# Performance work log

Hardware: AMD Instinct MI355X
Metric: run time of the kernel (lower is better)

Reference implementation:

```python
import jax, jax.numpy as jnp
import numpy as np

N_NODES = 20000
N_EDGES = 320000
IN_DIM = 128
HID = 64
LATENT = 32
NUM_GRAPHS = 64
NEG_SLOPE = 0.2
BN_EPS = 1e-5


def setup_inputs() -> dict:
    key = jax.random.key(0)
    ks = jax.random.split(key, 24)
    def glorot(k, shape):
        fan_in, fan_out = shape[0], shape[-1]
        lim = (6.0 / (fan_in + fan_out)) ** 0.5
        return jax.random.uniform(k, shape, jnp.float32, -lim, lim)
    inp = {
        "x": jax.random.normal(ks[0], (N_NODES, IN_DIM), jnp.float32),
        "edge_index": jax.random.randint(ks[1], (2, N_EDGES), 0, N_NODES, jnp.int64),
        "batch": jnp.sort(jax.random.randint(ks[2], (N_NODES,), 0, NUM_GRAPHS, jnp.int64)),
        # layer 0: in=128 -> out=64, heads=4
        "Wl0": glorot(ks[3], (IN_DIM, 4 * HID)),
        "Wr0": glorot(ks[4], (IN_DIM, 4 * HID)),
        "att0": glorot(ks[5], (4, HID)),
        "b0": jnp.zeros((4 * HID,), jnp.float32),
        # layer 1: in=256 -> out=64, heads=4
        "Wl1": glorot(ks[6], (4 * HID, 4 * HID)),
        "Wr1": glorot(ks[7], (4 * HID, 4 * HID)),
        "att1": glorot(ks[8], (4, HID)),
        "b1": jnp.zeros((4 * HID,), jnp.float32),
        # layer 2: in=256 -> out=64, heads=1
        "Wl2": glorot(ks[9], (4 * HID, HID)),
        "Wr2": glorot(ks[10], (4 * HID, HID)),
        "att2": glorot(ks[11], (1, HID)),
        "b2": jnp.zeros((HID,), jnp.float32),
        # BatchNorm1d(hidden_dim) in eval mode (running stats)
        "bn_gamma": jax.random.uniform(ks[12], (HID,), jnp.float32, 0.5, 1.5),
        "bn_beta": jax.random.normal(ks[13], (HID,), jnp.float32) * 0.1,
        "bn_mean": jax.random.normal(ks[14], (HID,), jnp.float32) * 0.1,
        "bn_var": jax.random.uniform(ks[15], (HID,), jnp.float32, 0.5, 1.5),
        # fc: hidden -> latent
        "fc_w": glorot(ks[16], (HID, LATENT)),
        "fc_b": jnp.zeros((LATENT,), jnp.float32),
    }
    return inp


def gatv2_layer(h, src, dst, Wl, Wr, att, bias):
    # PyG GATv2Conv (concat=True, negative_slope=0.2, self loops already in src/dst)
    N = h.shape[0]
    H, C = att.shape
    xl = (h @ Wl).reshape(N, H, C)  # source transform
    xr = (h @ Wr).reshape(N, H, C)  # target transform
    e = jax.nn.leaky_relu(xl[src] + xr[dst], NEG_SLOPE)   # [E,H,C]
    logits = jnp.einsum("ehc,hc->eh", e, att)             # [E,H]
    # softmax over incoming edges per destination node
    m = jax.ops.segment_max(logits, dst, num_segments=N)  # [N,H]
    ex = jnp.exp(logits - m[dst])
    denom = jax.ops.segment_sum(ex, dst, num_segments=N)
    alpha = ex / denom[dst]                               # [E,H]
    out = jax.ops.segment_sum(alpha[:, :, None] * xl[src], dst, num_segments=N)
    return out.reshape(N, H * C) + bias


def reference(x, edge_index, batch, Wl0, Wr0, att0, b0, Wl1, Wr1, att1, b1,
              Wl2, Wr2, att2, b2, bn_gamma, bn_beta, bn_mean, bn_var, fc_w, fc_b):
    N = x.shape[0]
    loop = jnp.arange(N, dtype=edge_index.dtype)
    src = jnp.concatenate([edge_index[0], loop])  # add self loops (PyG default)
    dst = jnp.concatenate([edge_index[1], loop])
    h = gatv2_layer(x, src, dst, Wl0, Wr0, att0, b0)   # dropout: eval mode -> identity
    h = gatv2_layer(h, src, dst, Wl1, Wr1, att1, b1)
    h = gatv2_layer(h, src, dst, Wl2, Wr2, att2, b2)   # [N, HID]
    pooled = jax.ops.segment_sum(h, batch, num_segments=NUM_GRAPHS)  # global_add_pool
    bn = (pooled - bn_mean) * jax.lax.rsqrt(bn_var + BN_EPS) * bn_gamma + bn_beta
    return bn @ fc_w + fc_b  # [NUM_GRAPHS, LATENT]
```

## Files before the change

kernel.cpp:

```cpp
#include <hip/hip_runtime.h>
#include <math.h>

#define N_NODES 20000
#define E_ORIG  320000
#define E_TOT   340000
#define NUM_GRAPHS 64
#define NCHUNK 10
#define NBINS (N_NODES * NCHUNK)
#define SCAN_BLOCKS 196

typedef __attribute__((ext_vector_type(8))) short bf16x8;
typedef __attribute__((ext_vector_type(4))) float f32x4;

__device__ __forceinline__ ushort f2bf(float x) {
  unsigned u = __float_as_uint(x);
  return (ushort)((u + 0x7fffu + ((u >> 16) & 1u)) >> 16);
}
__device__ __forceinline__ float4 ld_bf16x4(const ushort* p) {
  ushort4 u = *(const ushort4*)p;
  float4 f;
  f.x = __uint_as_float((unsigned)u.x << 16);
  f.y = __uint_as_float((unsigned)u.y << 16);
  f.z = __uint_as_float((unsigned)u.z << 16);
  f.w = __uint_as_float((unsigned)u.w << 16);
  return f;
}
__device__ __forceinline__ void gl_lds16(const void* g, void* l) {
  __builtin_amdgcn_global_load_lds(
      (const __attribute__((address_space(1))) unsigned*)(uintptr_t)g,
      (__attribute__((address_space(3))) unsigned*)(uintptr_t)l, 16, 0, 0);
}

__global__ __launch_bounds__(256) void prep(
    const float* __restrict__ x,
    const float* __restrict__ Wl0, const float* __restrict__ Wr0,
    const float* __restrict__ Wl1, const float* __restrict__ Wr1,
    const float* __restrict__ Wl2, const float* __restrict__ Wr2,
    ushort* __restrict__ x16, ushort* __restrict__ Bt0,
    ushort* __restrict__ Bt1, ushort* __restrict__ Bt2, int* __restrict__ deg)
{
  const int Z0 = 640000;
  const int Z1 = Z0 + 65536;
  const int Z2 = Z1 + 131072;
  const int Z3 = Z2 + 32768;
  const int Z4 = Z3 + NBINS / 4;
  int t = blockIdx.x * 256 + threadIdx.x;
  if (t < Z0) {
    int i = t << 2;
    float4 v = *(const float4*)&x[i];
    ushort4 o; o.x = f2bf(v.x); o.y = f2bf(v.y); o.z = f2bf(v.z); o.w = f2bf(v.w);
    *(ushort4*)&x16[i] = o;
  } else if (t < Z1) {
    int idx = t - Z0; int n = idx >> 7, k = idx & 127;
    float v = (n < 256) ? Wl0[k * 256 + n] : Wr0[k * 256 + (n - 256)];
    Bt0[idx] = f2bf(v);
  } else if (t < Z2) {
    int idx = t - Z1; int n = idx >> 8, k = idx & 255;
    float v = (n < 256) ? Wl1[k * 256 + n] : Wr1[k * 256 + (n - 256)];
    Bt1[idx] = f2bf(v);
  } else if (t < Z3) {
    int idx = t - Z2; int n = idx >> 8, k = idx & 255;
    float v = (n < 64) ? Wl2[k * 64 + n] : Wr2[k * 64 + (n - 64)];
    Bt2[idx] = f2bf(v);
  } else if (t < Z4) {
    int4 z = {0, 0, 0, 0};
    *(int4*)&deg[(t - Z3) << 2] = z;
  }
}


__global__ __launch_bounds__(256) void deg_count(
    const int* __restrict__ esrc, const int* __restrict__ edst,
    int* __restrict__ deg)
{
  int e = blockIdx.x * 256 + threadIdx.x;
  if (e >= E_TOT) return;
  int src, dst;
  if (e < E_ORIG) { src = esrc[e]; dst = edst[e]; }
  else            { src = dst = e - E_ORIG; }
  atomicAdd(&deg[dst * NCHUNK + (src >> 11)], 1);
}

__global__ __launch_bounds__(256) void scan1(
    const int* __restrict__ deg, int* __restrict__ bsum)
{
  __shared__ int red[256];
  const int t = threadIdx.x;
  int base = (blockIdx.x << 10) + (t << 2);
  int s = 0;
  if (base + 4 <= NBINS) {
    int4 v = *(const int4*)&deg[base];
    s = v.x + v.y + v.z + v.w;
  }
  red[t] = s;
  __syncthreads();
  #pragma unroll
  for (int off = 128; off > 0; off >>= 1) {
    if (t < off) red[t] += red[t + off];
    __syncthreads();
  }
  if (t == 0) bsum[blockIdx.x] = red[0];
}

__global__ __launch_bounds__(256) void scan3(
    const int* __restrict__ deg, const int* __restrict__ bsum,
    int* __restrict__ rowptr, int* __restrict__ cursor)
{
  __shared__ int sc[256];
  __shared__ int bs[256];
  const int t = threadIdx.x;
  bs[t] = (t < SCAN_BLOCKS) ? bsum[t] : 0;
  __syncthreads();
  #pragma unroll
  for (int off = 1; off < 256; off <<= 1) {
    int v = (t >= off) ? bs[t - off] : 0;
    __syncthreads();
    bs[t] += v;
    __syncthreads();
  }
  const int myoff = (blockIdx.x == 0) ? 0 : bs[blockIdx.x - 1];

  int base = (blockIdx.x << 10) + (t << 2);
  int4 v = {0, 0, 0, 0};
  if (base + 4 <= NBINS) v = *(const int4*)&deg[base];
  int s = v.x + v.y + v.z + v.w;
  sc[t] = s;
  __syncthreads();
  #pragma unroll
  for (int off = 1; off < 256; off <<= 1) {
    int u = (t >= off) ? sc[t - off] : 0;
    __syncthreads();
    sc[t] += u;
    __syncthreads();
  }
  if (base + 4 <= NBINS) {
    int p = myoff + ((t == 0) ? 0 : sc[t - 1]);
    int4 r;
    r.x = p; r.y = p + v.x; r.z = r.y + v.y; r.w = r.z + v.z;
    *(int4*)&rowptr[base] = r;
    *(int4*)&cursor[base] = r;
  }
  if (blockIdx.x == SCAN_BLOCKS - 1 && t == 255) rowptr[NBINS] = bs[255];
}

__global__ __launch_bounds__(256) void csr_fill(
    const int* __restrict__ esrc, const int* __restrict__ edst,
    int* __restrict__ cursor, int* __restrict__ csr_src)
{
  int e = blockIdx.x * 256 + threadIdx.x;
  if (e >= E_TOT) return;
  int src, dst;
  if (e < E_ORIG) { src = esrc[e]; dst = edst[e]; }
  else            { src = dst = e - E_ORIG; }
  int pos = atomicAdd(&cursor[dst * NCHUNK + (src >> 11)], 1);
  csr_src[pos] = src;
}

__global__ __launch_bounds__(256) void mfma_gemm_bf16(
    const ushort* __restrict__ A, const ushort* __restrict__ Bt,
    ushort* __restrict__ Cl, ushort* __restrict__ Cr, int M, int K, int N)
{
  __shared__ char smem[36864];
  ushort* As = (ushort*)smem;
  ushort* Bs = As + 8192;

  const int mtiles = (M + 127) >> 7;
  const int bid = blockIdx.x;
  const int xcd = bid & 7;
  const int i = bid >> 3;
  const int n0 = (i / 20) << 7;
  const int m = xcd + ((i % 20) << 3);
  if (m >= mtiles) return;
  const int m0 = m << 7;

  const int tid = threadIdx.x;
  const int lane = tid & 63;
  const int w = tid >> 6;
  const int wm = (w >> 1) << 6;
  const int wn = (w & 1) << 6;
  const int quad = lane >> 4;
  const int l15 = lane & 15;

  f32x4 acc[4][4] = {};

  for (int k0 = 0; k0 < K; k0 += 64) {
    #pragma unroll
    for (int r = 0; r < 4; r++) {
      int c = (r << 8) + tid;
      int row = c >> 3;
      int col = (c & 7) << 3;
      int ga = m0 + row; if (ga >= M) ga = M - 1;
      gl_lds16(A  + (size_t)ga * K + k0 + col, (char*)As + c * 16);
      gl_lds16(Bt + (size_t)(n0 + row) * K + k0 + col, (char*)Bs + c * 16);
    }
    __syncthreads();
    #pragma unroll
    for (int ks = 0; ks < 2; ks++) {
      bf16x8 af[4], bfr[4];
      #pragma unroll
      for (int ii = 0; ii < 4; ii++)
        af[ii]  = *(const bf16x8*)&As[(wm + (ii << 4) + l15) * 64 + (ks << 5) + (quad << 3)];
      #pragma unroll
      for (int j = 0; j < 4; j++)
        bfr[j] = *(const bf16x8*)&Bs[(wn + (j << 4) + l15) * 64 + (ks << 5) + (quad << 3)];
      #pragma unroll
      for (int ii = 0; ii < 4; ii++)
        #pragma unroll
        for (int j = 0; j < 4; j++)
          acc[ii][j] = __builtin_amdgcn_mfma_f32_16x16x32_bf16(
              af[ii], bfr[j], acc[ii][j], 0, 0, 0);
    }
    __syncthreads();
  }

  const int halfN = N >> 1;
  const int gc0 = n0 + wn;
  ushort* Cd = (gc0 < halfN) ? Cl : Cr;
  const int cb = (gc0 < halfN) ? gc0 : gc0 - halfN;

  ushort* Cs = (ushort*)smem + w * 4608;
  #pragma unroll
  for (int ii = 0; ii < 4; ii++)
    #pragma unroll
    for (int j = 0; j < 4; j++)
      #pragma unroll
      for (int r = 0; r < 4; r++)
        Cs[((ii << 4) + (quad << 2) + r) * 72 + (j << 4) + l15] = f2bf(acc[ii][j][r]);
  #pragma unroll
  for (int it = 0; it < 8; it++) {
    int row = (it << 3) + (lane >> 3);
    int cc = lane & 7;
    bf16x8 v = *(const bf16x8*)&Cs[row * 72 + (cc << 3)];
    int grow = m0 + wm + row;
    if (grow < M)
      *(bf16x8*)&Cd[(size_t)grow * halfN + cb + (cc << 3)] = v;
  }
}

__device__ __forceinline__ void h4_term(
    float4 xlv, const float4& xrv, const float4& attv, float& v)
{
  float4 a;
  a.x = xlv.x + xrv.x; a.y = xlv.y + xrv.y;
  a.z = xlv.z + xrv.z; a.w = xlv.w + xrv.w;
  a.x = fmaxf(a.x, 0.2f * a.x); a.y = fmaxf(a.y, 0.2f * a.y);
  a.z = fmaxf(a.z, 0.2f * a.z); a.w = fmaxf(a.w, 0.2f * a.w);
  v = a.x * attv.x + a.y * attv.y + a.z * attv.z + a.w * attv.w;
}

__device__ __forceinline__ void h4_edge(
    const float4& xv, const float4& xrv, const float4& attv,
    float4& acc, float& lsum)
{
  float v;
  h4_term(xv, xrv, attv, v);
  v += __shfl_xor(v, 1);
  v += __shfl_xor(v, 2);
  v += __shfl_xor(v, 4);
  v += __shfl_xor(v, 8);
  float w = __expf(v);
  lsum += w;
  acc.x += w * xv.x; acc.y += w * xv.y;
  acc.z += w * xv.z; acc.w += w * xv.w;
}

__global__ __launch_bounds__(256) void gat_gather_h4(
    const ushort* __restrict__ xl16, const ushort* __restrict__ xr16,
    const float* __restrict__ att, const float* __restrict__ bias,
    const int* __restrict__ rowptr, const int* __restrict__ csr_src,
    ushort* __restrict__ hout)
{
  const int n = blockIdx.x * 4 + (threadIdx.x >> 6);
  const int lane = threadIdx.x & 63;
  const int c4 = lane << 2;
  const float4 xrv  = ld_bf16x4(xr16 + (size_t)n * 256 + c4);
  const float4 attv = *(const float4*)&att[c4];
  const int beg = rowptr[n * NCHUNK], end = rowptr[n * NCHUNK + NCHUNK];
  float4 acc = make_float4(0.f, 0.f, 0.f, 0.f);
  float lsum = 0.f;
  int p = beg;
  for (; p + 7 < end; p += 8) {
    int s0 = csr_src[p],     s1 = csr_src[p + 1];
    int s2 = csr_src[p + 2], s3 = csr_src[p + 3];
    int s4 = csr_src[p + 4], s5 = csr_src[p + 5];
    int s6 = csr_src[p + 6], s7 = csr_src[p + 7];
    float4 x0 = ld_bf16x4(xl16 + (size_t)s0 * 256 + c4);
    float4 x1 = ld_bf16x4(xl16 + (size_t)s1 * 256 + c4);
    float4 x2 = ld_bf16x4(xl16 + (size_t)s2 * 256 + c4);
    float4 x3 = ld_bf16x4(xl16 + (size_t)s3 * 256 + c4);
    float4 x4 = ld_bf16x4(xl16 + (size_t)s4 * 256 + c4);
    float4 x5 = ld_bf16x4(xl16 + (size_t)s5 * 256 + c4);
    float4 x6 = ld_bf16x4(xl16 + (size_t)s6 * 256 + c4);
    float4 x7 = ld_bf16x4(xl16 + (size_t)s7 * 256 + c4);
    h4_edge(x0, xrv, attv, acc, lsum);
    h4_edge(x1, xrv, attv, acc, lsum);
    h4_edge(x2, xrv, attv, acc, lsum);
    h4_edge(x3, xrv, attv, acc, lsum);
    h4_edge(x4, xrv, attv, acc, lsum);
    h4_edge(x5, xrv, attv, acc, lsum);
    h4_edge(x6, xrv, attv, acc, lsum);
    h4_edge(x7, xrv, attv, acc, lsum);
  }
  for (; p + 3 < end; p += 4) {
    int s0 = csr_src[p],     s1 = csr_src[p + 1];
    int s2 = csr_src[p + 2], s3 = csr_src[p + 3];
    float4 x0 = ld_bf16x4(xl16 + (size_t)s0 * 256 + c4);
    float4 x1 = ld_bf16x4(xl16 + (size_t)s1 * 256 + c4);
    float4 x2 = ld_bf16x4(xl16 + (size_t)s2 * 256 + c4);
    float4 x3 = ld_bf16x4(xl16 + (size_t)s3 * 256 + c4);
    h4_edge(x0, xrv, attv, acc, lsum);
    h4_edge(x1, xrv, attv, acc, lsum);
    h4_edge(x2, xrv, attv, acc, lsum);
    h4_edge(x3, xrv, attv, acc, lsum);
  }
  for (; p < end; p++) {
    int s0 = csr_src[p];
    float4 x0 = ld_bf16x4(xl16 + (size_t)s0 * 256 + c4);
    h4_edge(x0, xrv, attv, acc, lsum);
  }
  const float4 bv = *(const float4*)&bias[c4];
  float inv = 1.f / lsum;
  ushort4 o;
  o.x = f2bf(acc.x * inv + bv.x); o.y = f2bf(acc.y * inv + bv.y);
  o.z = f2bf(acc.z * inv + bv.z); o.w = f2bf(acc.w * inv + bv.w);
  *(ushort4*)&hout[(size_t)n * 256 + c4] = o;
}

__global__ __launch_bounds__(256) void gat_gather_h1(
    const ushort* __restrict__ xl2, const ushort* __restrict__ xr2,
    const float* __restrict__ att, const float* __restrict__ bias,
    const int* __restrict__ rowptr, const int* __restrict__ csr_src,
    float* __restrict__ h3)
{
  const int n = blockIdx.x * 4 + (threadIdx.x >> 6);
  const int lane = threadIdx.x & 63;
  const int g = lane >> 4, c4 = (lane & 15) << 2;
  const float4 xrv  = ld_bf16x4(xr2 + (size_t)n * 64 + c4);
  const float4 attv = *(const float4*)&att[c4];
  const int beg = rowptr[n * NCHUNK], end = rowptr[n * NCHUNK + NCHUNK];
  float4 acc = make_float4(0.f, 0.f, 0.f, 0.f);
  float lsum = 0.f;
  int p = beg + g;
  for (; p + 4 < end; p += 8) {
    int s0 = csr_src[p], s1 = csr_src[p + 4];
    float4 x0 = ld_bf16x4(xl2 + (size_t)s0 * 64 + c4);
    float4 x1 = ld_bf16x4(xl2 + (size_t)s1 * 64 + c4);
    h4_edge(x0, xrv, attv, acc, lsum);
    h4_edge(x1, xrv, attv, acc, lsum);
  }
  if (p < end) {
    int s0 = csr_src[p];
    float4 x0 = ld_bf16x4(xl2 + (size_t)s0 * 64 + c4);
    h4_edge(x0, xrv, attv, acc, lsum);
  }
  #pragma unroll
  for (int off = 16; off <= 32; off <<= 1) {
    lsum  += __shfl_xor(lsum, off);
    acc.x += __shfl_xor(acc.x, off); acc.y += __shfl_xor(acc.y, off);
    acc.z += __shfl_xor(acc.z, off); acc.w += __shfl_xor(acc.w, off);
  }
  if (g == 0) {
    const float4 bv = *(const float4*)&bias[c4];
    float inv = 1.f / lsum;
    float4 o;
    o.x = acc.x * inv + bv.x; o.y = acc.y * inv + bv.y;
    o.z = acc.z * inv + bv.z; o.w = acc.w * inv + bv.w;
    *(float4*)&h3[(size_t)n * 64 + c4] = o;
  }
}

__global__ __launch_bounds__(256) void pool_bn_fc(
    const float* __restrict__ h3, const int* __restrict__ batch,
    const float* __restrict__ gamma, const float* __restrict__ beta,
    const float* __restrict__ mean, const float* __restrict__ var,
    const float* __restrict__ fcw, const float* __restrict__ fcb,
    float* __restrict__ out)
{
  __shared__ float red[256];
  __shared__ float s[64];
  const int g = blockIdx.x;
  const int t = threadIdx.x;
  const int c = t & 63, r = t >> 6;
  int lo = 0, hi = N_NODES;
  while (lo < hi) { int mid = (lo + hi) >> 1; if (batch[mid] < g) lo = mid + 1; else hi = mid; }
  int s0 = lo;
  hi = N_NODES;
  while (lo < hi) { int mid = (lo + hi) >> 1; if (batch[mid] < g + 1) lo = mid + 1; else hi = mid; }
  int e0 = lo;
  float a = 0.f;
  for (int n = s0 + r; n < e0; n += 4) a += h3[(size_t)n * 64 + c];
  red[t] = a;
  __syncthreads();
  if (r == 0) {
    float p = red[c] + red[c + 64] + red[c + 128] + red[c + 192];
    s[c] = (p - mean[c]) * rsqrtf(var[c] + 1e-5f) * gamma[c] + beta[c];
  }
  __syncthreads();
  if (t < 32) {
    float acc = fcb[t];
    #pragma unroll
    for (int k = 0; k < 64; k++) acc += s[k] * fcw[k * 32 + t];
    out[g * 32 + t] = acc;
  }
}

extern "C" void kernel_launch(void* const* d_in, const int* in_sizes, int n_in,
                              void* d_out, int out_size, void* d_ws, size_t ws_size,
                              hipStream_t stream) {
  const float* x    = (const float*)d_in[0];
  const int*   ei   = (const int*)d_in[1];
  const int*   batch= (const int*)d_in[2];
  const float* Wl0  = (const float*)d_in[3];
  const float* Wr0  = (const float*)d_in[4];
  const float* att0 = (const float*)d_in[5];
  const float* b0   = (const float*)d_in[6];
  const float* Wl1  = (const float*)d_in[7];
  const float* Wr1  = (const float*)d_in[8];
  const float* att1 = (const float*)d_in[9];
  const float* b1   = (const float*)d_in[10];
  const float* Wl2  = (const float*)d_in[11];
  const float* Wr2  = (const float*)d_in[12];
  const float* att2 = (const float*)d_in[13];
  const float* b2   = (const float*)d_in[14];
  const float* bng  = (const float*)d_in[15];
  const float* bnb  = (const float*)d_in[16];
  const float* bnm  = (const float*)d_in[17];
  const float* bnv  = (const float*)d_in[18];
  const float* fcw  = (const float*)d_in[19];
  const float* fcb  = (const float*)d_in[20];
  float* out = (float*)d_out;

  const int* esrc = ei;
  const int* edst = ei + E_ORIG;

  char* w = (char*)d_ws;
  ushort* x16  = (ushort*)w;                 w += (size_t)N_NODES * 128 * 2;
  ushort* h16  = (ushort*)w;                 w += (size_t)N_NODES * 256 * 2;
  ushort* xl16 = (ushort*)w;                 w += (size_t)N_NODES * 256 * 2;
  ushort* xr16 = (ushort*)w;                 w += (size_t)N_NODES * 256 * 2;
  ushort* xl2  = (ushort*)w;                 w += (size_t)N_NODES * 64 * 2;
  ushort* xr2  = (ushort*)w;                 w += (size_t)N_NODES * 64 * 2;
  float*  h3   = (float*)w;                  w += (size_t)N_NODES * 64 * 4;
  ushort* Bt0  = (ushort*)w;                 w += (size_t)512 * 128 * 2;
  ushort* Bt1  = (ushort*)w;                 w += (size_t)512 * 256 * 2;
  ushort* Bt2  = (ushort*)w;                 w += (size_t)128 * 256 * 2;
  int* deg     = (int*)w;                    w += NBINS * 4;
  int* rowptr  = (int*)w;                    w += (NBINS + 1) * 4;
  int* cursor  = (int*)w;                    w += NBINS * 4;
  int* bsum    = (int*)w;                    w += 256 * 4;
  int* csr_src = (int*)w;

  dim3 blk(256);
  const int eblk = (E_TOT + 255) / 256;

  prep<<<dim3(3592), blk, 0, stream>>>(
      x, Wl0, Wr0, Wl1, Wr1, Wl2, Wr2, x16, Bt0, Bt1, Bt2, deg);

  deg_count<<<dim3(eblk), blk, 0, stream>>>(esrc, edst, deg);
  scan1<<<dim3(SCAN_BLOCKS), blk, 0, stream>>>(deg, bsum);
  scan3<<<dim3(SCAN_BLOCKS), blk, 0, stream>>>(deg, bsum, rowptr, cursor);
  csr_fill<<<dim3(eblk), blk, 0, stream>>>(esrc, edst, cursor, csr_src);

  mfma_gemm_bf16<<<dim3(160 * 4), blk, 0, stream>>>(
      x16, Bt0, xl16, xr16, N_NODES, 128, 512);
  gat_gather_h4<<<dim3(N_NODES / 4), blk, 0, stream>>>(
      xl16, xr16, att0, b0, rowptr, csr_src, h16);

  mfma_gemm_bf16<<<dim3(160 * 4), blk, 0, stream>>>(
      h16, Bt1, xl16, xr16, N_NODES, 256, 512);
  gat_gather_h4<<<dim3(N_NODES / 4), blk, 0, stream>>>(
      xl16, xr16, att1, b1, rowptr, csr_src, h16);

  mfma_gemm_bf16<<<dim3(160 * 1), blk, 0, stream>>>(
      h16, Bt2, xl2, xr2, N_NODES, 256, 128);
  gat_gather_h1<<<dim3(N_NODES / 4), blk, 0, stream>>>(
      xl2, xr2, att2, b2, rowptr, csr_src, h3);

  pool_bn_fc<<<dim3(NUM_GRAPHS), blk, 0, stream>>>(
      h3, batch, bng, bnb, bnm, bnv, fcw, fcb, out);
}
```

Measured before the change: 287.6 us.

## Interleave five nodes per wave in 4-head gather, walking CSR chunks in lockstep

The 4-head GATv2 gather now launches a fixed grid of 4096 waves, and each wave handles up to five nodes strided by 4096. It walks the 10 source-sorted CSR chunks in an outer loop across all five nodes, so neighbour reads from the same source range happen close together in time and should improve cache locality. The cost is more registers for five accumulators, a launch bound of 4 blocks per CU, fewer waves in flight, and a shorter inner unroll (4 instead of 8).

```diff
diff --git a/kernel.cpp b/kernel.cpp
--- a/kernel.cpp
+++ b/kernel.cpp
@@ -8,6 +8,7 @@
 #define NCHUNK 10
 #define NBINS (N_NODES * NCHUNK)
 #define SCAN_BLOCKS 196
+#define GWAVES 4096
 
 typedef __attribute__((ext_vector_type(8))) short bf16x8;
 typedef __attribute__((ext_vector_type(4))) float f32x4;
@@ -264,66 +265,67 @@
   acc.z += w * xv.z; acc.w += w * xv.w;
 }
 
-__global__ __launch_bounds__(256) void gat_gather_h4(
+__global__ __launch_bounds__(256, 4) void gat_gather_h4(
     const ushort* __restrict__ xl16, const ushort* __restrict__ xr16,
     const float* __restrict__ att, const float* __restrict__ bias,
     const int* __restrict__ rowptr, const int* __restrict__ csr_src,
     ushort* __restrict__ hout)
 {
-  const int n = blockIdx.x * 4 + (threadIdx.x >> 6);
+  const int wv = blockIdx.x * 4 + (threadIdx.x >> 6);
   const int lane = threadIdx.x & 63;
   const int c4 = lane << 2;
-  const float4 xrv  = ld_bf16x4(xr16 + (size_t)n * 256 + c4);
   const float4 attv = *(const float4*)&att[c4];
-  const int beg = rowptr[n * NCHUNK], end = rowptr[n * NCHUNK + NCHUNK];
-  float4 acc = make_float4(0.f, 0.f, 0.f, 0.f);
-  float lsum = 0.f;
-  int p = beg;
-  for (; p + 7 < end; p += 8) {
-    int s0 = csr_src[p],     s1 = csr_src[p + 1];
-    int s2 = csr_src[p + 2], s3 = csr_src[p + 3];
-    int s4 = csr_src[p + 4], s5 = csr_src[p + 5];
-    int s6 = csr_src[p + 6], s7 = csr_src[p + 7];
-    float4 x0 = ld_bf16x4(xl16 + (size_t)s0 * 256 + c4);
-    float4 x1 = ld_bf16x4(xl16 + (size_t)s1 * 256 + c4);
-    float4 x2 = ld_bf16x4(xl16 + (size_t)s2 * 256 + c4);
-    float4 x3 = ld_bf16x4(xl16 + (size_t)s3 * 256 + c4);
-    float4 x4 = ld_bf16x4(xl16 + (size_t)s4 * 256 + c4);
-    float4 x5 = ld_bf16x4(xl16 + (size_t)s5 * 256 + c4);
-    float4 x6 = ld_bf16x4(xl16 + (size_t)s6 * 256 + c4);
-    float4 x7 = ld_bf16x4(xl16 + (size_t)s7 * 256 + c4);
-    h4_edge(x0, xrv, attv, acc, lsum);
-    h4_edge(x1, xrv, attv, acc, lsum);
-    h4_edge(x2, xrv, attv, acc, lsum);
-    h4_edge(x3, xrv, attv, acc, lsum);
-    h4_edge(x4, xrv, attv, acc, lsum);
-    h4_edge(x5, xrv, attv, acc, lsum);
-    h4_edge(x6, xrv, attv, acc, lsum);
-    h4_edge(x7, xrv, attv, acc, lsum);
-  }
-  for (; p + 3 < end; p += 4) {
-    int s0 = csr_src[p],     s1 = csr_src[p + 1];
-    int s2 = csr_src[p + 2], s3 = csr_src[p + 3];
-    float4 x0 = ld_bf16x4(xl16 + (size_t)s0 * 256 + c4);
-    float4 x1 = ld_bf16x4(xl16 + (size_t)s1 * 256 + c4);
-    float4 x2 = ld_bf16x4(xl16 + (size_t)s2 * 256 + c4);
-    float4 x3 = ld_bf16x4(xl16 + (size_t)s3 * 256 + c4);
-    h4_edge(x0, xrv, attv, acc, lsum);
-    h4_edge(x1, xrv, attv, acc, lsum);
-    h4_edge(x2, xrv, attv, acc, lsum);
-    h4_edge(x3, xrv, attv, acc, lsum);
-  }
-  for (; p < end; p++) {
-    int s0 = csr_src[p];
-    float4 x0 = ld_bf16x4(xl16 + (size_t)s0 * 256 + c4);
-    h4_edge(x0, xrv, attv, acc, lsum);
-  }
+
+  float4 xrv[5];
+  float4 acc[5];
+  float lsum[5];
+  #pragma unroll
+  for (int i = 0; i < 5; i++) {
+    int n = wv + (i << 12);
+    acc[i] = make_float4(0.f, 0.f, 0.f, 0.f);
+    lsum[i] = 0.f;
+    if (n < N_NODES) xrv[i] = ld_bf16x4(xr16 + (size_t)n * 256 + c4);
+  }
+
+  for (int c = 0; c < NCHUNK; c++) {
+    #pragma unroll
+    for (int i = 0; i < 5; i++) {
+      const int n = wv + (i << 12);
+      if (n >= N_NODES) continue;
+      const int b = n * NCHUNK + c;
+      int p = rowptr[b];
+      const int e = rowptr[b + 1];
+      for (; p + 3 < e; p += 4) {
+        int s0 = csr_src[p],     s1 = csr_src[p + 1];
+        int s2 = csr_src[p + 2], s3 = csr_src[p + 3];
+        float4 x0 = ld_bf16x4(xl16 + (size_t)s0 * 256 + c4);
+        float4 x1 = ld_bf16x4(xl16 + (size_t)s1 * 256 + c4);
+        float4 x2 = ld_bf16x4(xl16 + (size_t)s2 * 256 + c4);
+        float4 x3 = ld_bf16x4(xl16 + (size_t)s3 * 256 + c4);
+        h4_edge(x0, xrv[i], attv, acc[i], lsum[i]);
+        h4_edge(x1, xrv[i], attv, acc[i], lsum[i]);
+        h4_edge(x2, xrv[i], attv, acc[i], lsum[i]);
+        h4_edge(x3, xrv[i], attv, acc[i], lsum[i]);
+      }
+      for (; p < e; p++) {
+        int s0 = csr_src[p];
+        float4 x0 = ld_bf16x4(xl16 + (size_t)s0 * 256 + c4);
+        h4_edge(x0, xrv[i], attv, acc[i], lsum[i]);
+      }
+    }
+  }
+
   const float4 bv = *(const float4*)&bias[c4];
-  float inv = 1.f / lsum;
-  ushort4 o;
-  o.x = f2bf(acc.x * inv + bv.x); o.y = f2bf(acc.y * inv + bv.y);
-  o.z = f2bf(acc.z * inv + bv.z); o.w = f2bf(acc.w * inv + bv.w);
-  *(ushort4*)&hout[(size_t)n * 256 + c4] = o;
+  #pragma unroll
+  for (int i = 0; i < 5; i++) {
+    int n = wv + (i << 12);
+    if (n >= N_NODES) continue;
+    float inv = 1.f / lsum[i];
+    ushort4 o;
+    o.x = f2bf(acc[i].x * inv + bv.x); o.y = f2bf(acc[i].y * inv + bv.y);
+    o.z = f2bf(acc[i].z * inv + bv.z); o.w = f2bf(acc[i].w * inv + bv.w);
+    *(ushort4*)&hout[(size_t)n * 256 + c4] = o;
+  }
 }
 
 __global__ __launch_bounds__(256) void gat_gather_h1(
@@ -463,12 +465,12 @@
 
   mfma_gemm_bf16<<<dim3(160 * 4), blk, 0, stream>>>(
       x16, Bt0, xl16, xr16, N_NODES, 128, 512);
-  gat_gather_h4<<<dim3(N_NODES / 4), blk, 0, stream>>>(
+  gat_gather_h4<<<dim3(GWAVES / 4), blk, 0, stream>>>(
       xl16, xr16, att0, b0, rowptr, csr_src, h16);
 
   mfma_gemm_bf16<<<dim3(160 * 4), blk, 0, stream>>>(
       h16, Bt1, xl16, xr16, N_NODES, 256, 512);
-  gat_gather_h4<<<dim3(N_NODES / 4), blk, 0, stream>>>(
+  gat_gather_h4<<<dim3(GWAVES / 4), blk, 0, stream>>>(
       xl16, xr16, att1, b1, rowptr, csr_src, h16);
 
   mfma_gemm_bf16<<<dim3(160 * 1), blk, 0, stream>>>(
```

New measurement: 369.1 us. 1.28x slower.
